# Kernel tuning notes

Hardware: AMD Instinct MI355X
Metric: run time of the kernel (lower is better)

The kernel has to match this reference:

```python
import jax, jax.numpy as jnp
import numpy as np

N, E, F_IN, HID, C = 50000, 800000, 512, 256, 64
K, ALPHA = 10, 0.1


def setup_inputs() -> dict:
    key = jax.random.key(0)
    ks = jax.random.split(key, 6)
    x = jax.random.normal(ks[0], (N, F_IN), dtype=jnp.float32)
    edge_index = jax.random.randint(ks[1], (2, E), 0, N, dtype=jnp.int64)
    W1 = jax.random.normal(ks[2], (F_IN, HID), dtype=jnp.float32) / np.sqrt(F_IN)
    b1 = jnp.zeros((HID,), dtype=jnp.float32)
    W2 = jax.random.normal(ks[3], (HID, C), dtype=jnp.float32) / np.sqrt(HID)
    b2 = jnp.zeros((C,), dtype=jnp.float32)
    return {"x": x, "W1": W1, "b1": b1, "W2": W2, "b2": b2, "edge_index": edge_index}


def reference(x, W1, b1, W2, b2, edge_index):
    # MLP (dropout is identity in eval mode)
    h = jax.nn.relu(x @ W1 + b1)
    h = h @ W2 + b2  # [N, C]

    n = x.shape[0]
    self_loops = jnp.arange(n, dtype=edge_index.dtype)
    row = jnp.concatenate([edge_index[0], self_loops])  # source nodes
    col = jnp.concatenate([edge_index[1], self_loops])  # target nodes

    # GCN symmetric normalization with self-loops (PyG gcn_norm)
    deg = jax.ops.segment_sum(jnp.ones_like(col, dtype=h.dtype), col, num_segments=n)
    dinv = jnp.where(deg > 0, jax.lax.rsqrt(jnp.maximum(deg, 1e-12)), 0.0)
    norm = (dinv[row] * dinv[col])[:, None]  # [E+N, 1]

    x0 = h

    def step(z, _):
        msg = z[row] * norm                                    # gather + scale
        agg = jax.ops.segment_sum(msg, col, num_segments=n)    # scatter-add
        return (1.0 - ALPHA) * agg + ALPHA * x0, None

    z, _ = jax.lax.scan(step, x0, None, length=K)
    return z
```

## Files before the change

kernel.cpp:

```cpp
#include <hip/hip_runtime.h>

#define N_NODES 50000
#define N_EDGES 800000
#define F_INDIM 512
#define HID     256
#define N_CLS   64
#define K_STEPS 10
#define ALPHA_V 0.1f

#define NPB 28
#define NPW 7
#define ECAP 1536

typedef __attribute__((ext_vector_type(8))) short short8;
typedef __attribute__((ext_vector_type(4))) float f32x4;
typedef __attribute__((ext_vector_type(4))) unsigned short ushort4v;

__device__ __forceinline__ unsigned short f2bf(float f) {
  unsigned u = __builtin_bit_cast(unsigned, f);
  unsigned r = (u + 0x7fffu + ((u >> 16) & 1u)) >> 16;
  return (unsigned short)r;
}
__device__ __forceinline__ float bflo(unsigned g) {
  return __builtin_bit_cast(float, g << 16);
}
__device__ __forceinline__ float bfhi(unsigned g) {
  return __builtin_bit_cast(float, g & 0xffff0000u);
}

#define GLOAD_LDS16(g, l)                                                        \
  __builtin_amdgcn_global_load_lds(                                              \
      (const __attribute__((address_space(1))) unsigned int*)(g),                \
      (__attribute__((address_space(3))) unsigned int*)(l), 16, 0, 0)

__global__ void detect_kernel(const int* __restrict__ eb, int* __restrict__ flag) {
  __shared__ int any;
  if (threadIdx.x == 0) any = 0;
  __syncthreads();
  for (int j = threadIdx.x; j < 1024; j += 256) {
    if (eb[2 * j + 1] != 0) atomicOr(&any, 1);
  }
  __syncthreads();
  if (threadIdx.x == 0) flag[0] = any ? 0 : 1;
}

__global__ void count_kernel(const int* __restrict__ eb, const int* __restrict__ flagp,
                             int* __restrict__ cnt) {
  int e = blockIdx.x * 256 + threadIdx.x;
  if (e >= N_EDGES) return;
  int sh = flagp[0];
  int c = eb[((size_t)(N_EDGES + e)) << sh];
  atomicAdd(&cnt[c], 1);
}

__global__ void scan1_kernel(const int* __restrict__ cnt, int* __restrict__ ptr,
                             int* __restrict__ bsum) {
  __shared__ int sm[256];
  int t = threadIdx.x;
  int i = blockIdx.x * 256 + t;
  int v = (i < N_NODES) ? cnt[i] : 0;
  sm[t] = v;
  __syncthreads();
  for (int off = 1; off < 256; off <<= 1) {
    int x = sm[t];
    if (t >= off) x += sm[t - off];
    __syncthreads();
    sm[t] = x;
    __syncthreads();
  }
  int incl = sm[t];
  if (i < N_NODES) ptr[i] = incl - v;
  if (t == 255) bsum[blockIdx.x] = incl;
}

__global__ void scan2_kernel(int* __restrict__ bsum, int nblk) {
  __shared__ int sm[256];
  int t = threadIdx.x;
  int v = (t < nblk) ? bsum[t] : 0;
  sm[t] = v;
  __syncthreads();
  for (int off = 1; off < 256; off <<= 1) {
    int x = sm[t];
    if (t >= off) x += sm[t - off];
    __syncthreads();
    sm[t] = x;
    __syncthreads();
  }
  int incl = sm[t];
  if (t < nblk) bsum[t] = incl - v;
}

__global__ void scan3_kernel(int* __restrict__ ptr, const int* __restrict__ bsum) {
  int i = blockIdx.x * 256 + threadIdx.x;
  if (i < N_NODES) ptr[i] += bsum[i >> 8];
  if (i == 0) ptr[N_NODES] = N_EDGES;
}

__global__ void dinv_kernel(const int* __restrict__ cnt, const int* __restrict__ ptr,
                            float* __restrict__ dinv, float* __restrict__ selfw,
                            int* __restrict__ cursor) {
  int i = blockIdx.x * 256 + threadIdx.x;
  if (i >= N_NODES) return;
  float di = rsqrtf((float)cnt[i] + 1.0f);
  dinv[i] = di;
  selfw[i] = (1.0f - ALPHA_V) * di * di;
  cursor[i] = ptr[i];
}

__global__ void fill_kernel(const int* __restrict__ eb, const int* __restrict__ flagp,
                            const float* __restrict__ dinv, int* __restrict__ cursor,
                            int2* __restrict__ epack) {
  int e = blockIdx.x * 256 + threadIdx.x;
  if (e >= N_EDGES) return;
  int sh = flagp[0];
  int r = eb[((size_t)e) << sh];
  int c = eb[((size_t)(N_EDGES + e)) << sh];
  int pos = atomicAdd(&cursor[c], 1);
  float w = (1.0f - ALPHA_V) * dinv[r] * dinv[c];
  epack[pos] = make_int2(r, __float_as_int(w));
}

__global__ void prep_w(const float* __restrict__ W1, const float* __restrict__ W2,
                       unsigned short* __restrict__ W1T, unsigned short* __restrict__ W2T) {
  int i = blockIdx.x * 256 + threadIdx.x;
  if (i < F_INDIM * HID) {
    int k = i >> 8, c = i & 255;
    W1T[(size_t)c * F_INDIM + k] = f2bf(W1[i]);
  }
  int j = i - F_INDIM * HID;
  if (j >= 0 && j < HID * N_CLS) {
    int k = j >> 6, c = j & 63;
    W2T[(size_t)c * HID + k] = f2bf(W2[j]);
  }
}

__global__ __launch_bounds__(256, 4) void gemm1_mfma(
    const float* __restrict__ A, const unsigned short* __restrict__ BT,
    const float* __restrict__ bias, unsigned short* __restrict__ H, int M) {
  __shared__ unsigned short Ab[2][64 * 32];
  __shared__ unsigned short Bb[2][128 * 32];
  const int t = threadIdx.x;
  const int wave = t >> 6, lane = t & 63;
  const int l15 = lane & 15, l4 = lane >> 4;
  const int row0 = blockIdx.x * 64, col0 = blockIdx.y * 128;

  f32x4 acc[8];
#pragma unroll
  for (int n = 0; n < 8; ++n) acc[n] = (f32x4)0.0f;

  const int NT = F_INDIM / 32;

  auto stageB = [&](int buf, int kt) {
#pragma unroll
    for (int i = 0; i < 2; ++i) {
      int row = wave * 32 + i * 16 + (lane >> 2);
      int g = lane & 3;
      int kg = g ^ ((row >> 1) & 3);
      const unsigned short* src = BT + (size_t)(col0 + row) * F_INDIM + kt * 32 + kg * 8;
      unsigned short* dst = &Bb[buf][(wave * 32 + i * 16) * 32];
      GLOAD_LDS16(src, dst);
    }
  };
  f32x4 ar[2];
  int arow[2], acol[2];
  auto loadA = [&](int kt) {
#pragma unroll
    for (int i = 0; i < 2; ++i) {
      int idx = wave * 512 + i * 256 + lane * 4;
      int row = idx >> 5;
      int col = idx & 31;
      arow[i] = row; acol[i] = col;
      int gr = row0 + row;
      if (gr > M - 1) gr = M - 1;
      ar[i] = *(const f32x4*)(A + (size_t)gr * F_INDIM + kt * 32 + col);
    }
  };
  auto writeA = [&](int buf) {
#pragma unroll
    for (int i = 0; i < 2; ++i) {
      int row = arow[i], col = acol[i];
      int g = col >> 3;
      int gp = g ^ ((row >> 1) & 3);
      ushort4v o;
#pragma unroll
      for (int j = 0; j < 4; ++j) o[j] = f2bf(ar[i][j]);
      *(ushort4v*)(&Ab[buf][row * 32 + gp * 8 + (col & 7)]) = o;
    }
  };
  auto compute = [&](int buf) {
    int rowA = wave * 16 + l15;
    short8 af = *(const short8*)(&Ab[buf][rowA * 32 + (l4 ^ ((rowA >> 1) & 3)) * 8]);
    short8 bf[8];
#pragma unroll
    for (int n = 0; n < 8; ++n) {
      int c = n * 16 + l15;
      bf[n] = *(const short8*)(&Bb[buf][c * 32 + (l4 ^ ((c >> 1) & 3)) * 8]);
    }
#pragma unroll
    for (int n = 0; n < 8; ++n)
      acc[n] = __builtin_amdgcn_mfma_f32_16x16x32_bf16(af, bf[n], acc[n], 0, 0, 0);
  };

  stageB(0, 0);
  loadA(0);
  writeA(0);
  __syncthreads();
#pragma unroll 4
  for (int kt = 0; kt < NT; ++kt) {
    int cur = kt & 1;
    if (kt + 1 < NT) {
      stageB(cur ^ 1, kt + 1);
      loadA(kt + 1);
    }
    compute(cur);
    if (kt + 1 < NT) writeA(cur ^ 1);
    __syncthreads();
  }

  float bv[8];
#pragma unroll
  for (int n = 0; n < 8; ++n) bv[n] = bias[col0 + n * 16 + l15];
#pragma unroll
  for (int i = 0; i < 4; ++i) {
    int grow = row0 + wave * 16 + l4 * 4 + i;
    if (grow >= M) continue;
#pragma unroll
    for (int n = 0; n < 8; ++n) {
      int gcol = col0 + n * 16 + l15;
      float v = fmaxf(acc[n][i] + bv[n], 0.0f);
      H[(size_t)grow * HID + gcol] = f2bf(v);
    }
  }
}

__global__ __launch_bounds__(256) void gemm2_mfma(
    const unsigned short* __restrict__ Hm, const unsigned short* __restrict__ BT,
    const float* __restrict__ bias, unsigned short* __restrict__ Ch,
    int roff, int M) {
  const int t = threadIdx.x;
  const int wave = t >> 6, lane = t & 63;
  const int l15 = lane & 15, l4 = lane >> 4;
  const int row0 = blockIdx.x * 64 + wave * 16;

  f32x4 acc[4];
#pragma unroll
  for (int n = 0; n < 4; ++n) acc[n] = (f32x4)0.0f;

  int gr = row0 + l15;
  if (gr > M - 1) gr = M - 1;
  const unsigned short* arow = Hm + (size_t)gr * HID + l4 * 8;

#pragma unroll
  for (int kt = 0; kt < HID / 32; ++kt) {
    short8 af = *(const short8*)(arow + kt * 32);
    short8 bf[4];
#pragma unroll
    for (int n = 0; n < 4; ++n)
      bf[n] = *(const short8*)(BT + (size_t)(n * 16 + l15) * HID + kt * 32 + l4 * 8);
#pragma unroll
    for (int n = 0; n < 4; ++n)
      acc[n] = __builtin_amdgcn_mfma_f32_16x16x32_bf16(af, bf[n], acc[n], 0, 0, 0);
  }

#pragma unroll
  for (int n = 0; n < 4; ++n) {
    int gcol = n * 16 + l15;
    float bv = bias[gcol];
#pragma unroll
    for (int i = 0; i < 4; ++i) {
      int grow = row0 + l4 * 4 + i;
      if (grow < M) {
        float v = acc[n][i] + bv;
        Ch[(size_t)(roff + grow) * N_CLS + gcol] = f2bf(v);
      }
    }
  }
}

template <bool LAST>
__global__ __launch_bounds__(256) void prop_step(
    const unsigned int* __restrict__ zin, const unsigned int* __restrict__ x0h,
    const float* __restrict__ selfw, const int* __restrict__ ptr,
    const int2* __restrict__ epack, unsigned int* __restrict__ zout,
    float* __restrict__ outf) {
  __shared__ int2 erec[ECAP];
  __shared__ int lptr[NPB + 1];
  __shared__ float lsw[NPB];

  const int tid = threadIdx.x;
  const int n0 = blockIdx.x * NPB;
  int nEnd = N_NODES - n0;
  if (nEnd > NPB) nEnd = NPB;

  if (tid <= nEnd) lptr[tid] = ptr[n0 + tid];
  if (tid < nEnd) lsw[tid] = selfw[n0 + tid];
  __syncthreads();
  const int base = lptr[0];
  const int cnt = lptr[nEnd] - base;
  for (int i = tid; i < cnt && i < ECAP; i += 256) erec[i] = epack[base + i];
  __syncthreads();

  const int wv = tid >> 6, lane = tid & 63;
  const int eg = lane >> 4, c4 = lane & 15;

  auto run = [&](auto getrec) {
    for (int ni = wv * NPW; ni < wv * NPW + NPW; ++ni) {
      if (ni >= nEnd) break;
      const int node = n0 + ni;
      float a0 = 0.f, a1 = 0.f, a2 = 0.f, a3 = 0.f;
      if (eg == 0) {
        uint2 zs = *(const uint2*)&zin[(size_t)node * 32 + 2 * c4];
        uint2 xs = *(const uint2*)&x0h[(size_t)node * 32 + 2 * c4];
        float sw = lsw[ni];
        a0 = fmaf(sw, bflo(zs.x), ALPHA_V * bflo(xs.x));
        a1 = fmaf(sw, bfhi(zs.x), ALPHA_V * bfhi(xs.x));
        a2 = fmaf(sw, bflo(zs.y), ALPHA_V * bflo(xs.y));
        a3 = fmaf(sw, bfhi(zs.y), ALPHA_V * bfhi(xs.y));
      }
      int e = lptr[ni] - base, e1 = lptr[ni + 1] - base;
      for (; e + 16 <= e1; e += 16) {
        int2 p[4];
#pragma unroll
        for (int j = 0; j < 4; ++j) p[j] = getrec(e + 4 * j + eg);
        uint2 g[4];
#pragma unroll
        for (int j = 0; j < 4; ++j)
          g[j] = *(const uint2*)&zin[(size_t)p[j].x * 32 + 2 * c4];
#pragma unroll
        for (int j = 0; j < 4; ++j) {
          float w = __int_as_float(p[j].y);
          a0 = fmaf(w, bflo(g[j].x), a0);
          a1 = fmaf(w, bfhi(g[j].x), a1);
          a2 = fmaf(w, bflo(g[j].y), a2);
          a3 = fmaf(w, bfhi(g[j].y), a3);
        }
      }
      if (e < e1) {
        int2 p[4];
        float m[4];
#pragma unroll
        for (int j = 0; j < 4; ++j) {
          int gi = e + 4 * j + eg;
          bool ok = gi < e1;
          p[j] = getrec(ok ? gi : e);
          m[j] = ok ? 1.0f : 0.0f;
        }
        uint2 g[4];
#pragma unroll
        for (int j = 0; j < 4; ++j)
          g[j] = *(const uint2*)&zin[(size_t)p[j].x * 32 + 2 * c4];
#pragma unroll
        for (int j = 0; j < 4; ++j) {
          float w = m[j] * __int_as_float(p[j].y);
          a0 = fmaf(w, bflo(g[j].x), a0);
          a1 = fmaf(w, bfhi(g[j].x), a1);
          a2 = fmaf(w, bflo(g[j].y), a2);
          a3 = fmaf(w, bfhi(g[j].y), a3);
        }
      }
      a0 += __shfl_xor(a0, 16); a0 += __shfl_xor(a0, 32);
      a1 += __shfl_xor(a1, 16); a1 += __shfl_xor(a1, 32);
      a2 += __shfl_xor(a2, 16); a2 += __shfl_xor(a2, 32);
      a3 += __shfl_xor(a3, 16); a3 += __shfl_xor(a3, 32);
      if (eg == 0) {
        if (LAST) {
          *(float4*)(outf + (size_t)node * 64 + 4 * c4) =
              make_float4(a0, a1, a2, a3);
        } else {
          uint2 o;
          o.x = (unsigned)f2bf(a0) | ((unsigned)f2bf(a1) << 16);
          o.y = (unsigned)f2bf(a2) | ((unsigned)f2bf(a3) << 16);
          *(uint2*)&zout[(size_t)node * 32 + 2 * c4] = o;
        }
      }
    }
  };

  if (cnt <= ECAP) {
    run([&](int i) { return erec[i]; });
  } else {
    run([&](int i) { return epack[base + i]; });
  }
}

extern "C" void kernel_launch(void* const* d_in, const int* in_sizes, int n_in,
                              void* d_out, int out_size, void* d_ws, size_t ws_size,
                              hipStream_t stream) {
  const float* x  = (const float*)d_in[0];
  const float* W1 = (const float*)d_in[1];
  const float* b1 = (const float*)d_in[2];
  const float* W2 = (const float*)d_in[3];
  const float* b2 = (const float*)d_in[4];
  const int*   eb = (const int*)d_in[5];
  float* out = (float*)d_out;

  char* ws = (char*)d_ws;
  size_t off = 0;
  auto alloc = [&](size_t bytes) -> void* {
    void* p = ws + off;
    off = (off + bytes + 255) & ~(size_t)255;
    return p;
  };

  int*   flagp  = (int*)alloc(256);
  int*   cnt    = (int*)alloc(N_NODES * sizeof(int));
  int*   ptr    = (int*)alloc((N_NODES + 1) * sizeof(int));
  int*   cursor = (int*)alloc(N_NODES * sizeof(int));
  int*   bsum   = (int*)alloc(256 * sizeof(int));
  float* dinv   = (float*)alloc(N_NODES * sizeof(float));
  float* selfw  = (float*)alloc(N_NODES * sizeof(float));
  int2*  epack  = (int2*)alloc((size_t)N_EDGES * sizeof(int2));
  unsigned short* W1T = (unsigned short*)alloc((size_t)HID * F_INDIM * sizeof(unsigned short));
  unsigned short* W2T = (unsigned short*)alloc((size_t)N_CLS * HID * sizeof(unsigned short));
  unsigned int* x0h = (unsigned int*)alloc((size_t)N_NODES * 32 * sizeof(unsigned int));
  unsigned int* z1  = (unsigned int*)alloc((size_t)N_NODES * 32 * sizeof(unsigned int));
  unsigned int* z2  = (unsigned int*)alloc((size_t)N_NODES * 32 * sizeof(unsigned int));

  int nchunks = 1;
  while (nchunks < 16) {
    size_t hbytes = (size_t)(N_NODES / nchunks) * HID * sizeof(unsigned short);
    if (off + hbytes <= ws_size) break;
    nchunks <<= 1;
  }
  int Mc = N_NODES / nchunks;
  unsigned short* h = (unsigned short*)alloc((size_t)Mc * HID * sizeof(unsigned short));

  hipMemsetAsync(cnt, 0, N_NODES * sizeof(int), stream);
  detect_kernel<<<1, 256, 0, stream>>>(eb, flagp);
  count_kernel<<<(N_EDGES + 255) / 256, 256, 0, stream>>>(eb, flagp, cnt);
  int nblk = (N_NODES + 255) / 256;
  scan1_kernel<<<nblk, 256, 0, stream>>>(cnt, ptr, bsum);
  scan2_kernel<<<1, 256, 0, stream>>>(bsum, nblk);
  scan3_kernel<<<nblk, 256, 0, stream>>>(ptr, bsum);
  dinv_kernel<<<nblk, 256, 0, stream>>>(cnt, ptr, dinv, selfw, cursor);
  fill_kernel<<<(N_EDGES + 255) / 256, 256, 0, stream>>>(eb, flagp, dinv, cursor, epack);
  prep_w<<<(F_INDIM * HID + HID * N_CLS + 255) / 256, 256, 0, stream>>>(W1, W2, W1T, W2T);

  for (int ci = 0; ci < nchunks; ++ci) {
    const float* Achunk = x + (size_t)ci * Mc * F_INDIM;
    dim3 g1((Mc + 63) / 64, HID / 128);
    gemm1_mfma<<<g1, 256, 0, stream>>>(Achunk, W1T, b1, h, Mc);
    dim3 g2((Mc + 63) / 64);
    gemm2_mfma<<<g2, 256, 0, stream>>>(h, W2T, b2,
        (unsigned short*)x0h, ci * Mc, Mc);
  }

  int pgrid = (N_NODES + NPB - 1) / NPB;
  const unsigned int* zin = x0h;
  unsigned int* zo[2] = {z1, z2};
  for (int s = 0; s < K_STEPS - 1; ++s) {
    unsigned int* zout = zo[s & 1];
    prop_step<false><<<pgrid, 256, 0, stream>>>(zin, x0h, selfw, ptr, epack, zout, nullptr);
    zin = zout;
  }
  prop_step<true><<<pgrid, 256, 0, stream>>>(zin, x0h, selfw, ptr, epack, nullptr, out);
}
```

Before: 358.2 us.

## Stage fp32 A tiles via direct global-to-LDS loads and convert in compute

The A operand of the first GEMM is no longer loaded into registers, converted to bf16 and written to LDS. Fp32 tiles are now copied straight into LDS with the async global-to-LDS path, using an XOR swizzle, and converted to bf16 when fragments are read. Synchronisation becomes explicit vmcnt waits plus raw barriers, so the next tile's loads stay in flight while the current tile computes, and the loop is fully unrolled. The cost is twice the LDS footprint for A, which may lower occupancy, plus conversion work repeated in the compute stage.

```diff
diff --git a/kernel.cpp b/kernel.cpp
--- a/kernel.cpp
+++ b/kernel.cpp
@@ -137,7 +137,7 @@
 __global__ __launch_bounds__(256, 4) void gemm1_mfma(
     const float* __restrict__ A, const unsigned short* __restrict__ BT,
     const float* __restrict__ bias, unsigned short* __restrict__ H, int M) {
-  __shared__ unsigned short Ab[2][64 * 32];
+  __shared__ float Af[2][64 * 32];
   __shared__ unsigned short Bb[2][128 * 32];
   const int t = threadIdx.x;
   const int wave = t >> 6, lane = t & 63;
@@ -161,35 +161,29 @@
       GLOAD_LDS16(src, dst);
     }
   };
-  f32x4 ar[2];
-  int arow[2], acol[2];
-  auto loadA = [&](int kt) {
+  auto stageA = [&](int buf, int kt) {
 #pragma unroll
     for (int i = 0; i < 2; ++i) {
-      int idx = wave * 512 + i * 256 + lane * 4;
-      int row = idx >> 5;
-      int col = idx & 31;
-      arow[i] = row; acol[i] = col;
+      int row = wave * 16 + i * 8 + (lane >> 3);
       int gr = row0 + row;
       if (gr > M - 1) gr = M - 1;
-      ar[i] = *(const f32x4*)(A + (size_t)gr * F_INDIM + kt * 32 + col);
-    }
-  };
-  auto writeA = [&](int buf) {
-#pragma unroll
-    for (int i = 0; i < 2; ++i) {
-      int row = arow[i], col = acol[i];
-      int g = col >> 3;
-      int gp = g ^ ((row >> 1) & 3);
-      ushort4v o;
-#pragma unroll
-      for (int j = 0; j < 4; ++j) o[j] = f2bf(ar[i][j]);
-      *(ushort4v*)(&Ab[buf][row * 32 + gp * 8 + (col & 7)]) = o;
+      int g = lane & 7;
+      int gp = g ^ (row & 7);
+      const float* src = A + (size_t)gr * F_INDIM + kt * 32 + gp * 4;
+      float* dst = &Af[buf][(wave * 16 + i * 8) * 32];
+      GLOAD_LDS16(src, dst);
     }
   };
   auto compute = [&](int buf) {
     int rowA = wave * 16 + l15;
-    short8 af = *(const short8*)(&Ab[buf][rowA * 32 + (l4 ^ ((rowA >> 1) & 3)) * 8]);
+    f32x4 a0 = *(const f32x4*)(&Af[buf][rowA * 32 + ((2 * l4 + 0) ^ (rowA & 7)) * 4]);
+    f32x4 a1 = *(const f32x4*)(&Af[buf][rowA * 32 + ((2 * l4 + 1) ^ (rowA & 7)) * 4]);
+    short8 af;
+#pragma unroll
+    for (int j = 0; j < 4; ++j) {
+      af[j] = (short)f2bf(a0[j]);
+      af[4 + j] = (short)f2bf(a1[j]);
+    }
     short8 bf[8];
 #pragma unroll
     for (int n = 0; n < 8; ++n) {
@@ -201,20 +195,21 @@
       acc[n] = __builtin_amdgcn_mfma_f32_16x16x32_bf16(af, bf[n], acc[n], 0, 0, 0);
   };
 
+  stageA(0, 0);
   stageB(0, 0);
-  loadA(0);
-  writeA(0);
-  __syncthreads();
-#pragma unroll 4
+#pragma unroll
   for (int kt = 0; kt < NT; ++kt) {
     int cur = kt & 1;
     if (kt + 1 < NT) {
+      stageA(cur ^ 1, kt + 1);
       stageB(cur ^ 1, kt + 1);
-      loadA(kt + 1);
-    }
+      asm volatile("s_waitcnt vmcnt(4)" ::: "memory");
+    } else {
+      asm volatile("s_waitcnt vmcnt(0)" ::: "memory");
+    }
+    __builtin_amdgcn_s_barrier();
     compute(cur);
-    if (kt + 1 < NT) writeA(cur ^ 1);
-    __syncthreads();
+    __builtin_amdgcn_s_barrier();
   }
 
   float bv[8];
```

Result: no change. 353.6 us (-1.3%).
